# Performance work log

Measured on AMD Instinct MI355X. Metric: run time of the kernel, lower is better.

## Reference

```python
import jax, jax.numpy as jnp
import numpy as np

N_NODES = 50000
NUM_FEATURES = 256
HIDDEN_DIM = 64
N_EDGES = 1000000
NEG_SLOPE = 0.2  # PyG GATConv default negative_slope
EPS = 1e-16      # PyG softmax denominator epsilon


def gat_conv(x, src, dst, W, a_src, a_dst, bias, num_nodes):
    """Single-head PyG-style GATConv with self-loops already included in (src, dst).

    x: [N, F_in]; W: [F_in, F_out]; a_src/a_dst: [F_out]; bias: [F_out].
    """
    h = x @ W                                   # [N, F_out]
    alpha_src = h @ a_src                       # [N]
    alpha_dst = h @ a_dst                       # [N]
    e = alpha_src[src] + alpha_dst[dst]         # [E]
    e = jnp.where(e >= 0, e, NEG_SLOPE * e)     # LeakyReLU
    # segment softmax over incoming edges of each destination node
    m = jax.ops.segment_max(e, dst, num_segments=num_nodes)   # [N]
    e = jnp.exp(e - m[dst])                                    # [E]
    s = jax.ops.segment_sum(e, dst, num_segments=num_nodes)   # [N]
    alpha = e / (s[dst] + EPS)                                 # [E]
    out = jax.ops.segment_sum(alpha[:, None] * h[src], dst, num_segments=num_nodes)
    return out + bias


def setup_inputs() -> dict:
    key = jax.random.key(0)
    ks = jax.random.split(key, 12)
    glorot = lambda k, shp: jax.random.normal(k, shp, jnp.float32) * np.sqrt(2.0 / sum(shp))
    return {
        "x": jax.random.normal(ks[0], (N_NODES, NUM_FEATURES), jnp.float32),
        "edge_index": jax.random.randint(ks[1], (2, N_EDGES), 0, N_NODES, jnp.int64),
        "W1": glorot(ks[2], (NUM_FEATURES, HIDDEN_DIM)),
        "a1_src": glorot(ks[3], (HIDDEN_DIM,)),
        "a1_dst": glorot(ks[4], (HIDDEN_DIM,)),
        "b1": jnp.zeros((HIDDEN_DIM,), jnp.float32),
        "W2": glorot(ks[5], (HIDDEN_DIM, HIDDEN_DIM)),
        "a2_src": glorot(ks[6], (HIDDEN_DIM,)),
        "a2_dst": glorot(ks[7], (HIDDEN_DIM,)),
        "b2": jnp.zeros((HIDDEN_DIM,), jnp.float32),
        "fc_w": glorot(ks[8], (2 * HIDDEN_DIM, 1)),
        "fc_b": jnp.zeros((1,), jnp.float32),
    }


def reference(x, edge_index, W1, a1_src, a1_dst, b1, W2, a2_src, a2_dst, b2, fc_w, fc_b):
    num_nodes = x.shape[0]
    src_e, dst_e = edge_index[0], edge_index[1]
    # PyG GATConv adds self-loops by default
    loops = jnp.arange(num_nodes, dtype=edge_index.dtype)
    src = jnp.concatenate([src_e, loops])
    dst = jnp.concatenate([dst_e, loops])

    h = jax.nn.relu(gat_conv(x, src, dst, W1, a1_src, a1_dst, b1, num_nodes))
    h = jax.nn.relu(gat_conv(h, src, dst, W2, a2_src, a2_dst, b2, num_nodes))

    # edge-wise rating prediction on the ORIGINAL edges (no self-loops)
    combined = jnp.concatenate([h[src_e], h[dst_e]], axis=1)  # [E, 2*hidden]
    return combined @ fc_w + fc_b                              # [E, 1]
```

## Files before the change

### kernel.cpp

```cpp
#include <hip/hip_runtime.h>
#include <hip/hip_bf16.h>
#include <hip/hip_fp16.h>

#define NEG_SLOPE 0.2f
#define SEPS 1e-16f
#define CAP 64
#define NB 128
#define BSHIFT 9
#define CH 4096

using f16x8 = __attribute__((ext_vector_type(8))) _Float16;
using f32x4 = __attribute__((ext_vector_type(4))) float;

template <int K, bool HALF_IN>
__device__ __forceinline__ void gemm_body(char* smem, const void* __restrict__ Xv,
                                          const float* __restrict__ W,
                                          const float* __restrict__ av,
                                          const float* __restrict__ bv,
                                          __half* __restrict__ Yh,
                                          float* __restrict__ oa,
                                          float* __restrict__ ob, int N, int bid) {
  constexpr int PITCH = 40;
  _Float16* Al  = (_Float16*)smem;
  _Float16* Btl = Al + 64 * PITCH;
  _Float16* Ep  = (_Float16*)smem;

  int tid = threadIdx.x;
  int wid = tid >> 6, lane = tid & 63;
  int g = lane >> 4, c = lane & 15;
  int row0 = bid * 64;
  int sr = tid >> 2, sq = tid & 3;
  int wk = tid >> 4, wq = tid & 15;
  bool arow_ok = (row0 + sr) < N;
  const char* aptr = HALF_IN ? (const char*)((const _Float16*)Xv + (size_t)(row0 + sr) * K + sq * 8)
                             : (const char*)((const float*)Xv + (size_t)(row0 + sr) * K + sq * 8);

  f32x4 acc[4];
#pragma unroll
  for (int n = 0; n < 4; ++n) acc[n] = f32x4{0.f, 0.f, 0.f, 0.f};

  auto loadA = [&](int kt) -> f16x8 {
    f16x8 h = {};
    if (arow_ok) {
      if (HALF_IN) {
        h = *(const f16x8*)(aptr + (size_t)kt * 2);
      } else {
        const float* xp = (const float*)(aptr + (size_t)kt * 4);
        float4 a = *(const float4*)xp;
        float4 b = *(const float4*)(xp + 4);
        h[0] = (_Float16)a.x; h[1] = (_Float16)a.y;
        h[2] = (_Float16)a.z; h[3] = (_Float16)a.w;
        h[4] = (_Float16)b.x; h[5] = (_Float16)b.y;
        h[6] = (_Float16)b.z; h[7] = (_Float16)b.w;
      }
    }
    return h;
  };

  f16x8 ha = loadA(0);
  float4 w0 = *(const float4*)&W[(size_t)wk * 64 + wq * 4];
  float4 w1 = *(const float4*)&W[(size_t)(wk + 16) * 64 + wq * 4];

  for (int kt = 0; kt < K; kt += 32) {
    *(f16x8*)&Al[sr * PITCH + sq * 8] = ha;
    Btl[(wq * 4 + 0) * PITCH + wk] = (_Float16)w0.x;
    Btl[(wq * 4 + 1) * PITCH + wk] = (_Float16)w0.y;
    Btl[(wq * 4 + 2) * PITCH + wk] = (_Float16)w0.z;
    Btl[(wq * 4 + 3) * PITCH + wk] = (_Float16)w0.w;
    Btl[(wq * 4 + 0) * PITCH + wk + 16] = (_Float16)w1.x;
    Btl[(wq * 4 + 1) * PITCH + wk + 16] = (_Float16)w1.y;
    Btl[(wq * 4 + 2) * PITCH + wk + 16] = (_Float16)w1.z;
    Btl[(wq * 4 + 3) * PITCH + wk + 16] = (_Float16)w1.w;
    __syncthreads();
    f16x8 ha_n = {};
    float4 w0_n, w1_n;
    if (kt + 32 < K) {
      ha_n = loadA(kt + 32);
      w0_n = *(const float4*)&W[(size_t)(kt + 32 + wk) * 64 + wq * 4];
      w1_n = *(const float4*)&W[(size_t)(kt + 32 + wk + 16) * 64 + wq * 4];
    }
    f16x8 af = *(f16x8*)&Al[(wid * 16 + c) * PITCH + g * 8];
#pragma unroll
    for (int n = 0; n < 4; ++n) {
      f16x8 bf = *(f16x8*)&Btl[(n * 16 + c) * PITCH + g * 8];
      acc[n] = __builtin_amdgcn_mfma_f32_16x16x32_f16(af, bf, acc[n], 0, 0, 0);
    }
    __syncthreads();
    ha = ha_n; w0 = w0_n; w1 = w1_n;
  }

  {
    float avc[4], bvc[4];
#pragma unroll
    for (int n = 0; n < 4; ++n) { avc[n] = av[n * 16 + c]; bvc[n] = bv[n * 16 + c]; }
#pragma unroll
    for (int r = 0; r < 4; ++r) {
      float pa = 0.f, pb = 0.f;
#pragma unroll
      for (int n = 0; n < 4; ++n) { pa += acc[n][r] * avc[n]; pb += acc[n][r] * bvc[n]; }
#pragma unroll
      for (int off = 1; off < 16; off <<= 1) {
        pa += __shfl_xor(pa, off);
        pb += __shfl_xor(pb, off);
      }
      int row = row0 + wid * 16 + g * 4 + r;
      if (c == 0 && row < N) { oa[row] = pa; ob[row] = pb; }
    }
  }

  __syncthreads();
#pragma unroll
  for (int n = 0; n < 4; ++n)
#pragma unroll
    for (int r = 0; r < 4; ++r)
      Ep[(wid * 16 + g * 4 + r) * 72 + n * 16 + c] = (_Float16)acc[n][r];
  __syncthreads();
  {
    int row = row0 + sr;
    if (row < N) {
      float4 v0 = *(float4*)&Ep[sr * 72 + sq * 8];
      float4 v1 = *(float4*)&Ep[sr * 72 + (sq + 4) * 8];
      ((float4*)(Yh + (size_t)row * 64))[sq] = v0;
      ((float4*)(Yh + (size_t)row * 64))[sq + 4] = v1;
    }
  }
}

__device__ __forceinline__ void partition_body(char* smem, const void* ei,
                                               unsigned* __restrict__ bdata,
                                               int* __restrict__ pbh,
                                               int* __restrict__ plofs,
                                               unsigned* __restrict__ epk,
                                               int* __restrict__ cnt,
                                               int E, int N, int NPB, int pb) {
  int* hist = (int*)smem;
  int* lofs = hist + NB;
  unsigned* stage = (unsigned*)(lofs + NB);
  int* s_is64 = (int*)(stage + CH);
  int tid = threadIdx.x;
  long long Etot = (long long)E + N;
  long long base = (long long)pb * CH;

  for (int i = pb * 256 + tid; i < N; i += NPB * 256) cnt[i] = 0;
  if (tid < 64) {
    unsigned hi = ((const unsigned*)ei)[2 * tid + 1];
    unsigned long long m = __ballot(hi != 0);
    if (tid == 0) *s_is64 = (m == 0ULL) ? 1 : 0;
  }
  for (int i = tid; i < NB; i += 256) hist[i] = 0;
  __syncthreads();
  int f = *s_is64;

  unsigned sd[16];
  int lp[16], bk[16];
#pragma unroll
  for (int k = 0; k < 16; ++k) {
    long long i = base + tid + k * 256;
    if (i < Etot) {
      int s, d;
      if (i < E) {
        s = f ? (int)((const long long*)ei)[i] : ((const int*)ei)[i];
        d = f ? (int)((const long long*)ei)[E + i] : ((const int*)ei)[E + i];
      } else {
        s = d = (int)(i - E);
      }
      sd[k] = ((unsigned)d << 16) | (unsigned)s;
      bk[k] = d >> BSHIFT;
      lp[k] = atomicAdd(&hist[bk[k]], 1);
      if (i < E) epk[i] = sd[k];
    } else {
      bk[k] = -1;
    }
  }
  __syncthreads();
  if (tid < 64) {
    int h0 = hist[2 * tid], h1 = hist[2 * tid + 1];
    int v = h0 + h1, incl = v;
#pragma unroll
    for (int off = 1; off < 64; off <<= 1) {
      int t = __shfl_up(incl, off);
      if (tid >= off) incl += t;
    }
    int excl = incl - v;
    lofs[2 * tid] = excl;
    lofs[2 * tid + 1] = excl + h0;
  }
  __syncthreads();
  if (tid < NB) {
    pbh[pb * NB + tid] = hist[tid];
    plofs[pb * NB + tid] = lofs[tid];
  }
#pragma unroll
  for (int k = 0; k < 16; ++k)
    if (bk[k] >= 0) stage[lofs[bk[k]] + lp[k]] = sd[k];
  __syncthreads();
  int cnt_here = (int)((Etot - base < CH) ? (Etot - base) : CH);
  for (int j = tid; j < cnt_here; j += 256) bdata[base + j] = stage[j];
}

__global__ __launch_bounds__(256) void fused_front(const float* __restrict__ x,
                                                   const float* __restrict__ W1,
                                                   const float* __restrict__ a1s,
                                                   const float* __restrict__ a1d,
                                                   __half* __restrict__ hA,
                                                   float* __restrict__ alpha_s,
                                                   float* __restrict__ alpha_d,
                                                   const void* ei, unsigned* __restrict__ bdata,
                                                   int* __restrict__ pbh, int* __restrict__ plofs,
                                                   unsigned* __restrict__ epk,
                                                   int* __restrict__ cnt,
                                                   int E, int N, int NPB, int GB) {
  __shared__ __align__(16) char smem[(NB + NB) * 4 + CH * 4 + 16];
  if ((int)blockIdx.x < GB)
    gemm_body<256, false>(smem, x, W1, a1s, a1d, hA, alpha_s, alpha_d, N, blockIdx.x);
  else
    partition_body(smem, ei, bdata, pbh, plofs, epk, cnt, E, N, NPB, blockIdx.x - GB);
}

template <int K, bool HALF_IN>
__global__ __launch_bounds__(256) void gemm_mfma(const void* __restrict__ Xv,
                                                 const float* __restrict__ W,
                                                 const float* __restrict__ av,
                                                 const float* __restrict__ bv,
                                                 __half* __restrict__ Yh,
                                                 float* __restrict__ oa,
                                                 float* __restrict__ ob, int N) {
  __shared__ __align__(16) char smem[10240];
  gemm_body<K, HALF_IN>(smem, Xv, W, av, bv, Yh, oa, ob, N, blockIdx.x);
}

__global__ void build_kernel(const int* __restrict__ pbh, const int* __restrict__ plofs,
                             const unsigned* __restrict__ bdata, int* __restrict__ cnt,
                             unsigned short* __restrict__ csr, int NPB, int nb) {
  int b = blockIdx.x >> 2, sub = blockIdx.x & 3;
  if (b >= nb) return;
  __shared__ int cbase[66];
  __shared__ int cstart[67];
  int tid = threadIdx.x;
  int nj = (NPB - sub + 3) >> 2;
  if (tid < nj) {
    int B = sub + 4 * tid;
    cbase[tid] = B * CH + plofs[B * NB + b];
    cstart[tid] = pbh[B * NB + b];
  }
  __syncthreads();
  if (tid == 0) {
    int acc = 0;
    for (int j = 0; j < nj; ++j) { int l = cstart[j]; cstart[j] = acc; acc += l; }
    cstart[nj] = acc;
  }
  __syncthreads();
  int T = cstart[nj];
  for (int fidx = tid; fidx < T; fidx += 256) {
    int lo = 0, hi = nj;
    while (hi - lo > 1) {
      int mid = (lo + hi) >> 1;
      if (cstart[mid] <= fidx) lo = mid; else hi = mid;
    }
    unsigned v = bdata[cbase[lo] + (fidx - cstart[lo])];
    int d = (int)(v >> 16);
    int pos = atomicAdd(&cnt[d], 1);
    if (pos < CAP) csr[(size_t)d * CAP + pos] = (unsigned short)(v & 0xFFFFu);
  }
}

__global__ void agg_kernel(const int* __restrict__ cnt, const unsigned short* __restrict__ csr,
                           const __half* __restrict__ H, const float* __restrict__ as_,
                           const float* __restrict__ ad_, const float* __restrict__ bias,
                           __half* __restrict__ out, int N,
                           const float* __restrict__ pw,
                           float* __restrict__ pout, float* __restrict__ qout) {
  int node = (int)((blockIdx.x * blockDim.x + threadIdx.x) >> 6);
  int lane = threadIdx.x & 63;
  if (node >= N) return;
  int deg = cnt[node];
  deg = (deg > CAP) ? CAP : deg;
  const unsigned short* row = csr + (size_t)node * CAP;
  float ad = ad_[node];
  int g = lane >> 3, fl = lane & 7;
  int nj = (deg > g) ? ((deg - g + 7) >> 3) : 0;
  const float4* H16 = (const float4*)H;

  int sv[8];
#pragma unroll
  for (int j = 0; j < 8; ++j) sv[j] = row[j * 8 + g];
  float ev[8];
  float4 raw[8];
#pragma unroll
  for (int j = 0; j < 8; ++j)
    if (j < nj) ev[j] = as_[sv[j]];
#pragma unroll
  for (int j = 0; j < 8; ++j)
    if (j < nj) raw[j] = H16[(size_t)sv[j] * 8 + fl];

  float a[8];
#pragma unroll
  for (int k = 0; k < 8; ++k) a[k] = 0.f;
  float ss = 0.f;
#pragma unroll
  for (int j = 0; j < 8; ++j) {
    if (j < nj) {
      float e = ev[j] + ad;
      e = (e >= 0.f) ? e : NEG_SLOPE * e;
      float p = __expf(e);
      ss += p;
      float2 f0 = __half22float2(*(__half2*)&raw[j].x);
      float2 f1 = __half22float2(*(__half2*)&raw[j].y);
      float2 f2 = __half22float2(*(__half2*)&raw[j].z);
      float2 f3 = __half22float2(*(__half2*)&raw[j].w);
      a[0] += p * f0.x; a[1] += p * f0.y;
      a[2] += p * f1.x; a[3] += p * f1.y;
      a[4] += p * f2.x; a[5] += p * f2.y;
      a[6] += p * f3.x; a[7] += p * f3.y;
    }
  }
#pragma unroll
  for (int off = 8; off <= 32; off <<= 1) {
#pragma unroll
    for (int k = 0; k < 8; ++k) a[k] += __shfl_xor(a[k], off);
    ss += __shfl_xor(ss, off);
  }
  float inv = 1.f / (ss + SEPS);
  float o[8];
#pragma unroll
  for (int k = 0; k < 8; ++k) o[k] = fmaxf(a[k] * inv + bias[8 * fl + k], 0.f);
  if (g == 0) {
    if (out) {
      float4 packed;
      *(__half2*)&packed.x = __floats2half2_rn(o[0], o[1]);
      *(__half2*)&packed.y = __floats2half2_rn(o[2], o[3]);
      *(__half2*)&packed.z = __floats2half2_rn(o[4], o[5]);
      *(__half2*)&packed.w = __floats2half2_rn(o[6], o[7]);
      ((float4*)out)[(size_t)node * 8 + fl] = packed;
    }
    if (pw) {
      float pp = 0.f, qq = 0.f;
#pragma unroll
      for (int k = 0; k < 8; ++k) {
        pp += o[k] * pw[8 * fl + k];
        qq += o[k] * pw[64 + 8 * fl + k];
      }
#pragma unroll
      for (int off = 1; off < 8; off <<= 1) {
        pp += __shfl_xor(pp, off);
        qq += __shfl_xor(qq, off);
      }
      if (fl == 0) { pout[node] = pp; qout[node] = qq; }
    }
  }
}

__global__ void final_kernel(const unsigned* __restrict__ epk,
                             const float* __restrict__ p, const float* __restrict__ q,
                             const float* __restrict__ fcb, float* __restrict__ out,
                             int E, long long T) {
  long long t = (long long)blockIdx.x * blockDim.x + threadIdx.x;
  if (t >= T) return;
  float c = fcb[0];
#pragma unroll
  for (int k = 0; k < 4; ++k) {
    long long i = t + (long long)k * T;
    if (i < E) {
      unsigned v = epk[i];
      out[i] = p[v & 0xFFFFu] + q[v >> 16] + c;
    }
  }
}

extern "C" void kernel_launch(void* const* d_in, const int* in_sizes, int n_in,
                              void* d_out, int out_size, void* d_ws, size_t ws_size,
                              hipStream_t stream) {
  const float* x   = (const float*)d_in[0];
  const void*  ei  = d_in[1];
  const float* W1  = (const float*)d_in[2];
  const float* a1s = (const float*)d_in[3];
  const float* a1d = (const float*)d_in[4];
  const float* b1  = (const float*)d_in[5];
  const float* W2  = (const float*)d_in[6];
  const float* a2s = (const float*)d_in[7];
  const float* a2d = (const float*)d_in[8];
  const float* b2  = (const float*)d_in[9];
  const float* fcw = (const float*)d_in[10];
  const float* fcb = (const float*)d_in[11];
  float* out = (float*)d_out;

  int N = in_sizes[0] / 256;
  int E = in_sizes[1] / 2;
  long long Etot = (long long)E + N;
  int nb = (N + ((1 << BSHIFT) - 1)) >> BSHIFT;
  int NPB = (int)((Etot + CH - 1) / CH);
  int GB = (N + 63) / 64;

  char* w = (char*)d_ws;
  auto alloc = [&](size_t bytes) {
    char* p = w;
    w += (bytes + 255) & ~(size_t)255;
    return p;
  };
  int*            cnt     = (int*)alloc((size_t)N * 4);
  unsigned*       bdata   = (unsigned*)alloc((size_t)NPB * CH * 4);
  int*            pbh     = (int*)alloc((size_t)NPB * NB * 4);
  int*            plofs   = (int*)alloc((size_t)NPB * NB * 4);
  unsigned*       epk     = (unsigned*)alloc((size_t)E * 4);
  unsigned short* csr     = (unsigned short*)alloc((size_t)N * CAP * 2);
  float*          alpha_s = (float*)alloc((size_t)N * 4);
  float*          alpha_d = (float*)alloc((size_t)N * 4);
  __half*         hA      = (__half*)alloc((size_t)N * 64 * 2);
  __half*         hB      = (__half*)alloc((size_t)N * 64 * 2);
  float*          pbuf    = (float*)alloc((size_t)N * 4);
  float*          qbuf    = (float*)alloc((size_t)N * 4);

  fused_front<<<GB + NPB, 256, 0, stream>>>(x, W1, a1s, a1d, hA, alpha_s, alpha_d,
                                            ei, bdata, pbh, plofs, epk, cnt, E, N, NPB, GB);
  build_kernel<<<nb * 4, 256, 0, stream>>>(pbh, plofs, bdata, cnt, csr, NPB, nb);
  agg_kernel<<<(N + 3) / 4, 256, 0, stream>>>(cnt, csr, hA, alpha_s, alpha_d, b1, hB, N,
                                              nullptr, nullptr, nullptr);
  gemm_mfma<64, true><<<GB, 256, 0, stream>>>(hB, W2, a2s, a2d, hA, alpha_s, alpha_d, N);
  agg_kernel<<<(N + 3) / 4, 256, 0, stream>>>(cnt, csr, hA, alpha_s, alpha_d, b2, nullptr, N,
                                              fcw, pbuf, qbuf);
  long long T4 = ((long long)E + 3) / 4;
  final_kernel<<<(int)((T4 + 255) / 256), 256, 0, stream>>>(epk, pbuf, qbuf, fcb, out, E, T4);
}
```

Baseline: 122.5 us.

## Fuse layer-1 aggregation with layer-2 GEMM and widen final kernel per-thread work

Layer-1 neighbour aggregation now writes each 64-node tile into shared memory, and the same block multiplies it by W2 with MFMA to produce layer-2 features and attention logits. This removes a kernel launch and the global write and read of the intermediate hidden features. Separate alpha buffers are added because the fused kernel reads the layer-1 logits while writing the layer-2 ones. The trade-off is lower parallelism: the fused kernel launches one block per 64 nodes, and each wave aggregates 16 nodes in sequence, which may hide gather latency less well. The final edge kernel also processes 8 edges per thread instead of 4.

Measured after the change: 127.7 us. +4.3%, slower.

```diff
diff --git a/kernel.cpp b/kernel.cpp
--- a/kernel.cpp
+++ b/kernel.cpp
@@ -217,18 +217,6 @@
     partition_body(smem, ei, bdata, pbh, plofs, epk, cnt, E, N, NPB, blockIdx.x - GB);
 }
 
-template <int K, bool HALF_IN>
-__global__ __launch_bounds__(256) void gemm_mfma(const void* __restrict__ Xv,
-                                                 const float* __restrict__ W,
-                                                 const float* __restrict__ av,
-                                                 const float* __restrict__ bv,
-                                                 __half* __restrict__ Yh,
-                                                 float* __restrict__ oa,
-                                                 float* __restrict__ ob, int N) {
-  __shared__ __align__(16) char smem[10240];
-  gemm_body<K, HALF_IN>(smem, Xv, W, av, bv, Yh, oa, ob, N, blockIdx.x);
-}
-
 __global__ void build_kernel(const int* __restrict__ pbh, const int* __restrict__ plofs,
                              const unsigned* __restrict__ bdata, int* __restrict__ cnt,
                              unsigned short* __restrict__ csr, int NPB, int nb) {
@@ -264,23 +252,14 @@
   }
 }
 
-__global__ void agg_kernel(const int* __restrict__ cnt, const unsigned short* __restrict__ csr,
-                           const __half* __restrict__ H, const float* __restrict__ as_,
-                           const float* __restrict__ ad_, const float* __restrict__ bias,
-                           __half* __restrict__ out, int N,
-                           const float* __restrict__ pw,
-                           float* __restrict__ pout, float* __restrict__ qout) {
-  int node = (int)((blockIdx.x * blockDim.x + threadIdx.x) >> 6);
-  int lane = threadIdx.x & 63;
-  if (node >= N) return;
-  int deg = cnt[node];
-  deg = (deg > CAP) ? CAP : deg;
-  const unsigned short* row = csr + (size_t)node * CAP;
-  float ad = ad_[node];
-  int g = lane >> 3, fl = lane & 7;
+__device__ __forceinline__ void agg_node(int node, int deg,
+                                         const unsigned short* __restrict__ row,
+                                         const __half* __restrict__ H,
+                                         const float* __restrict__ as_, float ad,
+                                         const float* __restrict__ bias,
+                                         int g, int fl, float* o) {
   int nj = (deg > g) ? ((deg - g + 7) >> 3) : 0;
   const float4* H16 = (const float4*)H;
-
   int sv[8];
 #pragma unroll
   for (int j = 0; j < 8; ++j) sv[j] = row[j * 8 + g];
@@ -321,32 +300,135 @@
     ss += __shfl_xor(ss, off);
   }
   float inv = 1.f / (ss + SEPS);
+#pragma unroll
+  for (int k = 0; k < 8; ++k) o[k] = fmaxf(a[k] * inv + bias[8 * fl + k], 0.f);
+}
+
+__global__ __launch_bounds__(256) void agg_gemm(const int* __restrict__ cnt,
+                                                const unsigned short* __restrict__ csr,
+                                                const __half* __restrict__ H,
+                                                const float* __restrict__ as_,
+                                                const float* __restrict__ ad_,
+                                                const float* __restrict__ b1,
+                                                const float* __restrict__ W2,
+                                                const float* __restrict__ a2s,
+                                                const float* __restrict__ a2d,
+                                                __half* __restrict__ hA2,
+                                                float* __restrict__ oa2,
+                                                float* __restrict__ ob2, int N) {
+  constexpr int PITCH = 72;
+  __shared__ __align__(16) _Float16 Atile[64 * PITCH];
+  __shared__ __align__(16) _Float16 Btl[64 * PITCH];
+  int tid = threadIdx.x;
+  int wid = tid >> 6, lane = tid & 63;
+  int g = lane >> 3, fl = lane & 7;
+  int g4 = lane >> 4, c = lane & 15;
+  int base = blockIdx.x * 64;
+  int wk = tid >> 4, wq = tid & 15;
+
+#pragma unroll
+  for (int kk = 0; kk < 64; kk += 16) {
+    float4 w = *(const float4*)&W2[(size_t)(kk + wk) * 64 + wq * 4];
+    Btl[(wq * 4 + 0) * PITCH + kk + wk] = (_Float16)w.x;
+    Btl[(wq * 4 + 1) * PITCH + kk + wk] = (_Float16)w.y;
+    Btl[(wq * 4 + 2) * PITCH + kk + wk] = (_Float16)w.z;
+    Btl[(wq * 4 + 3) * PITCH + kk + wk] = (_Float16)w.w;
+  }
+
+  for (int t = 0; t < 16; ++t) {
+    int node = base + wid * 16 + t;
+    int nd = (node < N) ? node : 0;
+    int deg = (node < N) ? cnt[nd] : 0;
+    deg = (deg > CAP) ? CAP : deg;
+    float ad = ad_[nd];
+    float o[8];
+    agg_node(nd, deg, csr + (size_t)nd * CAP, H, as_, ad, b1, g, fl, o);
+    if (g == 0) {
+      f16x8 h;
+#pragma unroll
+      for (int k = 0; k < 8; ++k) h[k] = (node < N) ? (_Float16)o[k] : (_Float16)0.f;
+      *(f16x8*)&Atile[(wid * 16 + t) * PITCH + fl * 8] = h;
+    }
+  }
+  __syncthreads();
+
+  f32x4 acc[4];
+#pragma unroll
+  for (int n = 0; n < 4; ++n) acc[n] = f32x4{0.f, 0.f, 0.f, 0.f};
+#pragma unroll
+  for (int kt = 0; kt < 64; kt += 32) {
+    f16x8 af = *(f16x8*)&Atile[(wid * 16 + c) * PITCH + kt + g4 * 8];
+#pragma unroll
+    for (int n = 0; n < 4; ++n) {
+      f16x8 bf = *(f16x8*)&Btl[(n * 16 + c) * PITCH + kt + g4 * 8];
+      acc[n] = __builtin_amdgcn_mfma_f32_16x16x32_f16(af, bf, acc[n], 0, 0, 0);
+    }
+  }
+
+  {
+    float avc[4], bvc[4];
+#pragma unroll
+    for (int n = 0; n < 4; ++n) { avc[n] = a2s[n * 16 + c]; bvc[n] = a2d[n * 16 + c]; }
+#pragma unroll
+    for (int r = 0; r < 4; ++r) {
+      float pa = 0.f, pb = 0.f;
+#pragma unroll
+      for (int n = 0; n < 4; ++n) { pa += acc[n][r] * avc[n]; pb += acc[n][r] * bvc[n]; }
+#pragma unroll
+      for (int off = 1; off < 16; off <<= 1) {
+        pa += __shfl_xor(pa, off);
+        pb += __shfl_xor(pb, off);
+      }
+      int row = base + wid * 16 + g4 * 4 + r;
+      if (c == 0 && row < N) { oa2[row] = pa; ob2[row] = pb; }
+    }
+  }
+
+  __syncthreads();
+#pragma unroll
+  for (int n = 0; n < 4; ++n)
+#pragma unroll
+    for (int r = 0; r < 4; ++r)
+      Atile[(wid * 16 + g4 * 4 + r) * PITCH + n * 16 + c] = (_Float16)acc[n][r];
+  __syncthreads();
+  {
+    int sr = tid >> 2, sq = tid & 3;
+    int row = base + sr;
+    if (row < N) {
+      float4 v0 = *(float4*)&Atile[sr * PITCH + sq * 8];
+      float4 v1 = *(float4*)&Atile[sr * PITCH + (sq + 4) * 8];
+      ((float4*)(hA2 + (size_t)row * 64))[sq] = v0;
+      ((float4*)(hA2 + (size_t)row * 64))[sq + 4] = v1;
+    }
+  }
+}
+
+__global__ void agg2_kernel(const int* __restrict__ cnt, const unsigned short* __restrict__ csr,
+                            const __half* __restrict__ H, const float* __restrict__ as_,
+                            const float* __restrict__ ad_, const float* __restrict__ bias,
+                            int N, const float* __restrict__ pw,
+                            float* __restrict__ pout, float* __restrict__ qout) {
+  int node = (int)((blockIdx.x * blockDim.x + threadIdx.x) >> 6);
+  int lane = threadIdx.x & 63;
+  if (node >= N) return;
+  int deg = cnt[node];
+  deg = (deg > CAP) ? CAP : deg;
+  int g = lane >> 3, fl = lane & 7;
   float o[8];
-#pragma unroll
-  for (int k = 0; k < 8; ++k) o[k] = fmaxf(a[k] * inv + bias[8 * fl + k], 0.f);
+  agg_node(node, deg, csr + (size_t)node * CAP, H, as_, ad_[node], bias, g, fl, o);
   if (g == 0) {
-    if (out) {
-      float4 packed;
-      *(__half2*)&packed.x = __floats2half2_rn(o[0], o[1]);
-      *(__half2*)&packed.y = __floats2half2_rn(o[2], o[3]);
-      *(__half2*)&packed.z = __floats2half2_rn(o[4], o[5]);
-      *(__half2*)&packed.w = __floats2half2_rn(o[6], o[7]);
-      ((float4*)out)[(size_t)node * 8 + fl] = packed;
-    }
-    if (pw) {
-      float pp = 0.f, qq = 0.f;
-#pragma unroll
-      for (int k = 0; k < 8; ++k) {
-        pp += o[k] * pw[8 * fl + k];
-        qq += o[k] * pw[64 + 8 * fl + k];
-      }
-#pragma unroll
-      for (int off = 1; off < 8; off <<= 1) {
-        pp += __shfl_xor(pp, off);
-        qq += __shfl_xor(qq, off);
-      }
-      if (fl == 0) { pout[node] = pp; qout[node] = qq; }
-    }
+    float pp = 0.f, qq = 0.f;
+#pragma unroll
+    for (int k = 0; k < 8; ++k) {
+      pp += o[k] * pw[8 * fl + k];
+      qq += o[k] * pw[64 + 8 * fl + k];
+    }
+#pragma unroll
+    for (int off = 1; off < 8; off <<= 1) {
+      pp += __shfl_xor(pp, off);
+      qq += __shfl_xor(qq, off);
+    }
+    if (fl == 0) { pout[node] = pp; qout[node] = qq; }
   }
 }
 
@@ -358,7 +440,7 @@
   if (t >= T) return;
   float c = fcb[0];
 #pragma unroll
-  for (int k = 0; k < 4; ++k) {
+  for (int k = 0; k < 8; ++k) {
     long long i = t + (long long)k * T;
     if (i < E) {
       unsigned v = epk[i];
@@ -397,27 +479,28 @@
     w += (bytes + 255) & ~(size_t)255;
     return p;
   };
-  int*            cnt     = (int*)alloc((size_t)N * 4);
-  unsigned*       bdata   = (unsigned*)alloc((size_t)NPB * CH * 4);
-  int*            pbh     = (int*)alloc((size_t)NPB * NB * 4);
-  int*            plofs   = (int*)alloc((size_t)NPB * NB * 4);
-  unsigned*       epk     = (unsigned*)alloc((size_t)E * 4);
-  unsigned short* csr     = (unsigned short*)alloc((size_t)N * CAP * 2);
-  float*          alpha_s = (float*)alloc((size_t)N * 4);
-  float*          alpha_d = (float*)alloc((size_t)N * 4);
-  __half*         hA      = (__half*)alloc((size_t)N * 64 * 2);
-  __half*         hB      = (__half*)alloc((size_t)N * 64 * 2);
-  float*          pbuf    = (float*)alloc((size_t)N * 4);
-  float*          qbuf    = (float*)alloc((size_t)N * 4);
+  int*            cnt      = (int*)alloc((size_t)N * 4);
+  unsigned*       bdata    = (unsigned*)alloc((size_t)NPB * CH * 4);
+  int*            pbh      = (int*)alloc((size_t)NPB * NB * 4);
+  int*            plofs    = (int*)alloc((size_t)NPB * NB * 4);
+  unsigned*       epk      = (unsigned*)alloc((size_t)E * 4);
+  unsigned short* csr      = (unsigned short*)alloc((size_t)N * CAP * 2);
+  float*          alpha_s  = (float*)alloc((size_t)N * 4);
+  float*          alpha_d  = (float*)alloc((size_t)N * 4);
+  float*          alpha_s2 = (float*)alloc((size_t)N * 4);
+  float*          alpha_d2 = (float*)alloc((size_t)N * 4);
+  __half*         hA       = (__half*)alloc((size_t)N * 64 * 2);
+  __half*         hA2      = (__half*)alloc((size_t)N * 64 * 2);
+  float*          pbuf     = (float*)alloc((size_t)N * 4);
+  float*          qbuf     = (float*)alloc((size_t)N * 4);
 
   fused_front<<<GB + NPB, 256, 0, stream>>>(x, W1, a1s, a1d, hA, alpha_s, alpha_d,
                                             ei, bdata, pbh, plofs, epk, cnt, E, N, NPB, GB);
   build_kernel<<<nb * 4, 256, 0, stream>>>(pbh, plofs, bdata, cnt, csr, NPB, nb);
-  agg_kernel<<<(N + 3) / 4, 256, 0, stream>>>(cnt, csr, hA, alpha_s, alpha_d, b1, hB, N,
-                                              nullptr, nullptr, nullptr);
-  gemm_mfma<64, true><<<GB, 256, 0, stream>>>(hB, W2, a2s, a2d, hA, alpha_s, alpha_d, N);
-  agg_kernel<<<(N + 3) / 4, 256, 0, stream>>>(cnt, csr, hA, alpha_s, alpha_d, b2, nullptr, N,
-                                              fcw, pbuf, qbuf);
-  long long T4 = ((long long)E + 3) / 4;
-  final_kernel<<<(int)((T4 + 255) / 256), 256, 0, stream>>>(epk, pbuf, qbuf, fcb, out, E, T4);
-}
+  agg_gemm<<<GB, 256, 0, stream>>>(cnt, csr, hA, alpha_s, alpha_d, b1, W2, a2s, a2d,
+                                   hA2, alpha_s2, alpha_d2, N);
+  agg2_kernel<<<(N + 3) / 4, 256, 0, stream>>>(cnt, csr, hA2, alpha_s2, alpha_d2, b2, N,
+                                               fcw, pbuf, qbuf);
+  long long T8 = ((long long)E + 7) / 8;
+  final_kernel<<<(int)((T8 + 255) / 256), 256, 0, stream>>>(epk, pbuf, qbuf, fcb, out, E, T8);
+}
```

## Build CSR with one block per bucket using LDS degree counters

Applied to the files above, without the earlier changes.

The CSR build kernel now runs one block per destination bucket of 512 nodes instead of four sub-blocks, and counts degrees with LDS atomics in place of global atomics on cnt. Each block writes the capped counts at the end, so the cnt zeroing in the partition blocks is removed. A wave-level scan replaces the serial prefix sum, and each thread issues four bdata loads before doing the atomics. Separately, layer-2 alpha values go to their own buffers and the final kernel handles eight edges per thread. The cost is fewer build blocks (about 98), so less parallelism, and NPB must stay within MAXNPB=320 with PER at most 8.

After: 129.3 us. 5.6% more time.

```diff
diff --git a/kernel.cpp b/kernel.cpp
--- a/kernel.cpp
+++ b/kernel.cpp
@@ -8,6 +8,7 @@
 #define NB 128
 #define BSHIFT 9
 #define CH 4096
+#define MAXNPB 320
 
 using f16x8 = __attribute__((ext_vector_type(8))) _Float16;
 using f32x4 = __attribute__((ext_vector_type(4))) float;
@@ -131,8 +132,7 @@
                                                int* __restrict__ pbh,
                                                int* __restrict__ plofs,
                                                unsigned* __restrict__ epk,
-                                               int* __restrict__ cnt,
-                                               int E, int N, int NPB, int pb) {
+                                               int E, int N, int pb) {
   int* hist = (int*)smem;
   int* lofs = hist + NB;
   unsigned* stage = (unsigned*)(lofs + NB);
@@ -141,7 +141,6 @@
   long long Etot = (long long)E + N;
   long long base = (long long)pb * CH;
 
-  for (int i = pb * 256 + tid; i < N; i += NPB * 256) cnt[i] = 0;
   if (tid < 64) {
     unsigned hi = ((const unsigned*)ei)[2 * tid + 1];
     unsigned long long m = __ballot(hi != 0);
@@ -208,13 +207,12 @@
                                                    const void* ei, unsigned* __restrict__ bdata,
                                                    int* __restrict__ pbh, int* __restrict__ plofs,
                                                    unsigned* __restrict__ epk,
-                                                   int* __restrict__ cnt,
-                                                   int E, int N, int NPB, int GB) {
+                                                   int E, int N, int GB) {
   __shared__ __align__(16) char smem[(NB + NB) * 4 + CH * 4 + 16];
   if ((int)blockIdx.x < GB)
     gemm_body<256, false>(smem, x, W1, a1s, a1d, hA, alpha_s, alpha_d, N, blockIdx.x);
   else
-    partition_body(smem, ei, bdata, pbh, plofs, epk, cnt, E, N, NPB, blockIdx.x - GB);
+    partition_body(smem, ei, bdata, pbh, plofs, epk, E, N, blockIdx.x - GB);
 }
 
 template <int K, bool HALF_IN>
@@ -229,58 +227,95 @@
   gemm_body<K, HALF_IN>(smem, Xv, W, av, bv, Yh, oa, ob, N, blockIdx.x);
 }
 
-__global__ void build_kernel(const int* __restrict__ pbh, const int* __restrict__ plofs,
-                             const unsigned* __restrict__ bdata, int* __restrict__ cnt,
-                             unsigned short* __restrict__ csr, int NPB, int nb) {
-  int b = blockIdx.x >> 2, sub = blockIdx.x & 3;
-  if (b >= nb) return;
-  __shared__ int cbase[66];
-  __shared__ int cstart[67];
+__global__ __launch_bounds__(256) void build_kernel(const int* __restrict__ pbh,
+                                                    const int* __restrict__ plofs,
+                                                    const unsigned* __restrict__ bdata,
+                                                    int* __restrict__ cnt,
+                                                    unsigned short* __restrict__ csr,
+                                                    int NPB, int N) {
+  int b = blockIdx.x;
+  __shared__ int cbase[MAXNPB];
+  __shared__ int cstart[MAXNPB + 1];
+  __shared__ int lcnt[1 << BSHIFT];
   int tid = threadIdx.x;
-  int nj = (NPB - sub + 3) >> 2;
-  if (tid < nj) {
-    int B = sub + 4 * tid;
-    cbase[tid] = B * CH + plofs[B * NB + b];
-    cstart[tid] = pbh[B * NB + b];
-  }
-  __syncthreads();
-  if (tid == 0) {
-    int acc = 0;
-    for (int j = 0; j < nj; ++j) { int l = cstart[j]; cstart[j] = acc; acc += l; }
-    cstart[nj] = acc;
-  }
-  __syncthreads();
-  int T = cstart[nj];
-  for (int fidx = tid; fidx < T; fidx += 256) {
-    int lo = 0, hi = nj;
-    while (hi - lo > 1) {
-      int mid = (lo + hi) >> 1;
-      if (cstart[mid] <= fidx) lo = mid; else hi = mid;
-    }
-    unsigned v = bdata[cbase[lo] + (fidx - cstart[lo])];
-    int d = (int)(v >> 16);
-    int pos = atomicAdd(&cnt[d], 1);
-    if (pos < CAP) csr[(size_t)d * CAP + pos] = (unsigned short)(v & 0xFFFFu);
-  }
-}
-
-__global__ void agg_kernel(const int* __restrict__ cnt, const unsigned short* __restrict__ csr,
-                           const __half* __restrict__ H, const float* __restrict__ as_,
-                           const float* __restrict__ ad_, const float* __restrict__ bias,
-                           __half* __restrict__ out, int N,
-                           const float* __restrict__ pw,
-                           float* __restrict__ pout, float* __restrict__ qout) {
-  int node = (int)((blockIdx.x * blockDim.x + threadIdx.x) >> 6);
-  int lane = threadIdx.x & 63;
-  if (node >= N) return;
-  int deg = cnt[node];
-  deg = (deg > CAP) ? CAP : deg;
-  const unsigned short* row = csr + (size_t)node * CAP;
-  float ad = ad_[node];
-  int g = lane >> 3, fl = lane & 7;
+  for (int j = tid; j < NPB; j += 256) {
+    cbase[j] = j * CH + plofs[j * NB + b];
+    cstart[j] = pbh[j * NB + b];
+  }
+  for (int i = tid; i < (1 << BSHIFT); i += 256) lcnt[i] = 0;
+  __syncthreads();
+  if (tid < 64) {
+    const int PER = (NPB + 63) >> 6;
+    int idx0 = tid * PER;
+    int vals[8];
+    int lsum = 0;
+#pragma unroll 5
+    for (int k = 0; k < PER; ++k) {
+      int id = idx0 + k;
+      int v = (id < NPB) ? cstart[id] : 0;
+      vals[k] = lsum;
+      lsum += v;
+    }
+    int incl = lsum;
+#pragma unroll
+    for (int off = 1; off < 64; off <<= 1) {
+      int t = __shfl_up(incl, off);
+      if (tid >= off) incl += t;
+    }
+    int excl = incl - lsum;
+#pragma unroll 5
+    for (int k = 0; k < PER; ++k) {
+      int id = idx0 + k;
+      if (id < NPB) cstart[id] = excl + vals[k];
+    }
+    if (tid == 63) cstart[NPB] = incl;
+  }
+  __syncthreads();
+  int T = cstart[NPB];
+  int dbase = b << BSHIFT;
+  for (int it = tid; it < T; it += 1024) {
+    unsigned v[4];
+    int ok[4];
+#pragma unroll
+    for (int k = 0; k < 4; ++k) {
+      int fidx = it + k * 256;
+      ok[k] = fidx < T;
+      if (ok[k]) {
+        int lo = 0, hi = NPB;
+        while (hi - lo > 1) {
+          int mid = (lo + hi) >> 1;
+          if (cstart[mid] <= fidx) lo = mid; else hi = mid;
+        }
+        v[k] = bdata[cbase[lo] + (fidx - cstart[lo])];
+      }
+    }
+#pragma unroll
+    for (int k = 0; k < 4; ++k) {
+      if (ok[k]) {
+        int d = (int)(v[k] >> 16);
+        int pos = atomicAdd(&lcnt[d - dbase], 1);
+        if (pos < CAP) csr[(size_t)d * CAP + pos] = (unsigned short)(v[k] & 0xFFFFu);
+      }
+    }
+  }
+  __syncthreads();
+  for (int i = tid; i < (1 << BSHIFT); i += 256) {
+    int node = dbase + i;
+    if (node < N) {
+      int c = lcnt[i];
+      cnt[node] = (c > CAP) ? CAP : c;
+    }
+  }
+}
+
+__device__ __forceinline__ void agg_node(int deg,
+                                         const unsigned short* __restrict__ row,
+                                         const __half* __restrict__ H,
+                                         const float* __restrict__ as_, float ad,
+                                         const float* __restrict__ bias,
+                                         int g, int fl, float* o) {
   int nj = (deg > g) ? ((deg - g + 7) >> 3) : 0;
   const float4* H16 = (const float4*)H;
-
   int sv[8];
 #pragma unroll
   for (int j = 0; j < 8; ++j) sv[j] = row[j * 8 + g];
@@ -321,9 +356,23 @@
     ss += __shfl_xor(ss, off);
   }
   float inv = 1.f / (ss + SEPS);
+#pragma unroll
+  for (int k = 0; k < 8; ++k) o[k] = fmaxf(a[k] * inv + bias[8 * fl + k], 0.f);
+}
+
+__global__ void agg_kernel(const int* __restrict__ cnt, const unsigned short* __restrict__ csr,
+                           const __half* __restrict__ H, const float* __restrict__ as_,
+                           const float* __restrict__ ad_, const float* __restrict__ bias,
+                           __half* __restrict__ out, int N,
+                           const float* __restrict__ pw,
+                           float* __restrict__ pout, float* __restrict__ qout) {
+  int node = (int)((blockIdx.x * blockDim.x + threadIdx.x) >> 6);
+  int lane = threadIdx.x & 63;
+  if (node >= N) return;
+  int deg = cnt[node];
+  int g = lane >> 3, fl = lane & 7;
   float o[8];
-#pragma unroll
-  for (int k = 0; k < 8; ++k) o[k] = fmaxf(a[k] * inv + bias[8 * fl + k], 0.f);
+  agg_node(deg, csr + (size_t)node * CAP, H, as_, ad_[node], bias, g, fl, o);
   if (g == 0) {
     if (out) {
       float4 packed;
@@ -358,7 +407,7 @@
   if (t >= T) return;
   float c = fcb[0];
 #pragma unroll
-  for (int k = 0; k < 4; ++k) {
+  for (int k = 0; k < 8; ++k) {
     long long i = t + (long long)k * T;
     if (i < E) {
       unsigned v = epk[i];
@@ -397,27 +446,29 @@
     w += (bytes + 255) & ~(size_t)255;
     return p;
   };
-  int*            cnt     = (int*)alloc((size_t)N * 4);
-  unsigned*       bdata   = (unsigned*)alloc((size_t)NPB * CH * 4);
-  int*            pbh     = (int*)alloc((size_t)NPB * NB * 4);
-  int*            plofs   = (int*)alloc((size_t)NPB * NB * 4);
-  unsigned*       epk     = (unsigned*)alloc((size_t)E * 4);
-  unsigned short* csr     = (unsigned short*)alloc((size_t)N * CAP * 2);
-  float*          alpha_s = (float*)alloc((size_t)N * 4);
-  float*          alpha_d = (float*)alloc((size_t)N * 4);
-  __half*         hA      = (__half*)alloc((size_t)N * 64 * 2);
-  __half*         hB      = (__half*)alloc((size_t)N * 64 * 2);
-  float*          pbuf    = (float*)alloc((size_t)N * 4);
-  float*          qbuf    = (float*)alloc((size_t)N * 4);
+  int*            cnt      = (int*)alloc((size_t)N * 4);
+  unsigned*       bdata    = (unsigned*)alloc((size_t)NPB * CH * 4);
+  int*            pbh      = (int*)alloc((size_t)NPB * NB * 4);
+  int*            plofs    = (int*)alloc((size_t)NPB * NB * 4);
+  unsigned*       epk      = (unsigned*)alloc((size_t)E * 4);
+  unsigned short* csr      = (unsigned short*)alloc((size_t)N * CAP * 2);
+  float*          alpha_s  = (float*)alloc((size_t)N * 4);
+  float*          alpha_d  = (float*)alloc((size_t)N * 4);
+  float*          alpha_s2 = (float*)alloc((size_t)N * 4);
+  float*          alpha_d2 = (float*)alloc((size_t)N * 4);
+  __half*         hA       = (__half*)alloc((size_t)N * 64 * 2);
+  __half*         hB       = (__half*)alloc((size_t)N * 64 * 2);
+  float*          pbuf     = (float*)alloc((size_t)N * 4);
+  float*          qbuf     = (float*)alloc((size_t)N * 4);
 
   fused_front<<<GB + NPB, 256, 0, stream>>>(x, W1, a1s, a1d, hA, alpha_s, alpha_d,
-                                            ei, bdata, pbh, plofs, epk, cnt, E, N, NPB, GB);
-  build_kernel<<<nb * 4, 256, 0, stream>>>(pbh, plofs, bdata, cnt, csr, NPB, nb);
+                                            ei, bdata, pbh, plofs, epk, E, N, GB);
+  build_kernel<<<nb, 256, 0, stream>>>(pbh, plofs, bdata, cnt, csr, NPB, N);
   agg_kernel<<<(N + 3) / 4, 256, 0, stream>>>(cnt, csr, hA, alpha_s, alpha_d, b1, hB, N,
                                               nullptr, nullptr, nullptr);
-  gemm_mfma<64, true><<<GB, 256, 0, stream>>>(hB, W2, a2s, a2d, hA, alpha_s, alpha_d, N);
-  agg_kernel<<<(N + 3) / 4, 256, 0, stream>>>(cnt, csr, hA, alpha_s, alpha_d, b2, nullptr, N,
+  gemm_mfma<64, true><<<GB, 256, 0, stream>>>(hB, W2, a2s, a2d, hA, alpha_s2, alpha_d2, N);
+  agg_kernel<<<(N + 3) / 4, 256, 0, stream>>>(cnt, csr, hA, alpha_s2, alpha_d2, b2, nullptr, N,
                                               fcw, pbuf, qbuf);
-  long long T4 = ((long long)E + 3) / 4;
-  final_kernel<<<(int)((T4 + 255) / 256), 256, 0, stream>>>(epk, pbuf, qbuf, fcb, out, E, T4);
-}
+  long long T8 = ((long long)E + 7) / 8;
+  final_kernel<<<(int)((T8 + 255) / 256), 256, 0, stream>>>(epk, pbuf, qbuf, fcb, out, E, T8);
+}
```

## Split node features into two 32-wide half planes and restructure aggregation per plane

Applied to the files above, without the earlier changes.

Node feature matrices are now stored as two planes of 32 halves each (columns 0-31, then 32-63), written by the GEMM epilogue and read plane by plane in the aggregation kernel. The aggregation kernel now maps 16 edge groups of 4 lanes, loads the CSR row with ushort4 vector loads, and computes softmax weights once before gathering each plane. This is meant to make each gathered row segment smaller and more cache-friendly and to cut shuffle work. It also gives the second layer separate alpha buffers and has the final kernel handle 8 edges per thread. The cost is two passes of gathers and reductions per node.

Measured after the change: 173.1 us. 41.4% more time.

```diff
diff --git a/kernel.cpp b/kernel.cpp
--- a/kernel.cpp
+++ b/kernel.cpp
@@ -11,6 +11,7 @@
 
 using f16x8 = __attribute__((ext_vector_type(8))) _Float16;
 using f32x4 = __attribute__((ext_vector_type(4))) float;
+
 
 template <int K, bool HALF_IN>
 __device__ __forceinline__ void gemm_body(char* smem, const void* __restrict__ Xv,
@@ -32,8 +33,8 @@
   int sr = tid >> 2, sq = tid & 3;
   int wk = tid >> 4, wq = tid & 15;
   bool arow_ok = (row0 + sr) < N;
-  const char* aptr = HALF_IN ? (const char*)((const _Float16*)Xv + (size_t)(row0 + sr) * K + sq * 8)
-                             : (const char*)((const float*)Xv + (size_t)(row0 + sr) * K + sq * 8);
+  const float*    aptrF = (const float*)Xv + (size_t)(row0 + sr) * K + sq * 8;
+  const _Float16* aptrH = (const _Float16*)Xv + (size_t)(row0 + sr) * 32 + sq * 8;
 
   f32x4 acc[4];
 #pragma unroll
@@ -43,9 +44,9 @@
     f16x8 h = {};
     if (arow_ok) {
       if (HALF_IN) {
-        h = *(const f16x8*)(aptr + (size_t)kt * 2);
+        h = *(const f16x8*)(aptrH + (kt >= 32 ? (size_t)N * 32 : 0));
       } else {
-        const float* xp = (const float*)(aptr + (size_t)kt * 4);
+        const float* xp = aptrF + kt;
         float4 a = *(const float4*)xp;
         float4 b = *(const float4*)(xp + 4);
         h[0] = (_Float16)a.x; h[1] = (_Float16)a.y;
@@ -120,8 +121,8 @@
     if (row < N) {
       float4 v0 = *(float4*)&Ep[sr * 72 + sq * 8];
       float4 v1 = *(float4*)&Ep[sr * 72 + (sq + 4) * 8];
-      ((float4*)(Yh + (size_t)row * 64))[sq] = v0;
-      ((float4*)(Yh + (size_t)row * 64))[sq + 4] = v1;
+      ((float4*)(Yh + (size_t)row * 32))[sq] = v0;
+      ((float4*)(Yh + (size_t)N * 32 + (size_t)row * 32))[sq] = v1;
     }
   }
 }
@@ -265,7 +266,8 @@
 }
 
 __global__ void agg_kernel(const int* __restrict__ cnt, const unsigned short* __restrict__ csr,
-                           const __half* __restrict__ H, const float* __restrict__ as_,
+                           const __half* __restrict__ H,
+                           const float* __restrict__ as_,
                            const float* __restrict__ ad_, const float* __restrict__ bias,
                            __half* __restrict__ out, int N,
                            const float* __restrict__ pw,
@@ -277,76 +279,83 @@
   deg = (deg > CAP) ? CAP : deg;
   const unsigned short* row = csr + (size_t)node * CAP;
   float ad = ad_[node];
-  int g = lane >> 3, fl = lane & 7;
-  int nj = (deg > g) ? ((deg - g + 7) >> 3) : 0;
-  const float4* H16 = (const float4*)H;
-
-  int sv[8];
-#pragma unroll
-  for (int j = 0; j < 8; ++j) sv[j] = row[j * 8 + g];
-  float ev[8];
-  float4 raw[8];
-#pragma unroll
-  for (int j = 0; j < 8; ++j)
-    if (j < nj) ev[j] = as_[sv[j]];
-#pragma unroll
-  for (int j = 0; j < 8; ++j)
-    if (j < nj) raw[j] = H16[(size_t)sv[j] * 8 + fl];
-
-  float a[8];
-#pragma unroll
-  for (int k = 0; k < 8; ++k) a[k] = 0.f;
+  int g = lane >> 2, fl = lane & 3;
+  int nj = deg - g * 4;
+  nj = nj < 0 ? 0 : (nj > 4 ? 4 : nj);
+
+  ushort4 sv4 = *(const ushort4*)&row[g * 4];
+  int sv[4] = {sv4.x, sv4.y, sv4.z, sv4.w};
+
+  float p[4];
   float ss = 0.f;
 #pragma unroll
-  for (int j = 0; j < 8; ++j) {
+  for (int j = 0; j < 4; ++j) {
     if (j < nj) {
-      float e = ev[j] + ad;
+      float e = as_[sv[j]] + ad;
       e = (e >= 0.f) ? e : NEG_SLOPE * e;
-      float p = __expf(e);
-      ss += p;
-      float2 f0 = __half22float2(*(__half2*)&raw[j].x);
-      float2 f1 = __half22float2(*(__half2*)&raw[j].y);
-      float2 f2 = __half22float2(*(__half2*)&raw[j].z);
-      float2 f3 = __half22float2(*(__half2*)&raw[j].w);
-      a[0] += p * f0.x; a[1] += p * f0.y;
-      a[2] += p * f1.x; a[3] += p * f1.y;
-      a[4] += p * f2.x; a[5] += p * f2.y;
-      a[6] += p * f3.x; a[7] += p * f3.y;
-    }
-  }
-#pragma unroll
-  for (int off = 8; off <= 32; off <<= 1) {
-#pragma unroll
-    for (int k = 0; k < 8; ++k) a[k] += __shfl_xor(a[k], off);
-    ss += __shfl_xor(ss, off);
-  }
+      p[j] = __expf(e);
+      ss += p[j];
+    } else {
+      p[j] = 0.f;
+    }
+  }
+#pragma unroll
+  for (int off = 4; off <= 32; off <<= 1) ss += __shfl_xor(ss, off);
   float inv = 1.f / (ss + SEPS);
-  float o[8];
-#pragma unroll
-  for (int k = 0; k < 8; ++k) o[k] = fmaxf(a[k] * inv + bias[8 * fl + k], 0.f);
-  if (g == 0) {
-    if (out) {
+
+  float pp = 0.f, qq = 0.f;
+#pragma unroll
+  for (int h = 0; h < 2; ++h) {
+    const float4* H16 = (const float4*)(H + (size_t)h * N * 32);
+    float4 raw[4];
+#pragma unroll
+    for (int j = 0; j < 4; ++j)
+      if (j < nj) raw[j] = H16[(size_t)sv[j] * 4 + fl];
+    float a[8];
+#pragma unroll
+    for (int k = 0; k < 8; ++k) a[k] = 0.f;
+#pragma unroll
+    for (int j = 0; j < 4; ++j) {
+      if (j < nj) {
+        float2 f0 = __half22float2(*(__half2*)&raw[j].x);
+        float2 f1 = __half22float2(*(__half2*)&raw[j].y);
+        float2 f2 = __half22float2(*(__half2*)&raw[j].z);
+        float2 f3 = __half22float2(*(__half2*)&raw[j].w);
+        a[0] += p[j] * f0.x; a[1] += p[j] * f0.y;
+        a[2] += p[j] * f1.x; a[3] += p[j] * f1.y;
+        a[4] += p[j] * f2.x; a[5] += p[j] * f2.y;
+        a[6] += p[j] * f3.x; a[7] += p[j] * f3.y;
+      }
+    }
+#pragma unroll
+    for (int off = 4; off <= 32; off <<= 1) {
+#pragma unroll
+      for (int k = 0; k < 8; ++k) a[k] += __shfl_xor(a[k], off);
+    }
+    float o[8];
+#pragma unroll
+    for (int k = 0; k < 8; ++k)
+      o[k] = fmaxf(a[k] * inv + bias[h * 32 + fl * 8 + k], 0.f);
+    if (out && g == 0) {
       float4 packed;
       *(__half2*)&packed.x = __floats2half2_rn(o[0], o[1]);
       *(__half2*)&packed.y = __floats2half2_rn(o[2], o[3]);
       *(__half2*)&packed.z = __floats2half2_rn(o[4], o[5]);
       *(__half2*)&packed.w = __floats2half2_rn(o[6], o[7]);
-      ((float4*)out)[(size_t)node * 8 + fl] = packed;
+      ((float4*)(out + (size_t)h * N * 32 + (size_t)node * 32))[fl] = packed;
     }
     if (pw) {
-      float pp = 0.f, qq = 0.f;
 #pragma unroll
       for (int k = 0; k < 8; ++k) {
-        pp += o[k] * pw[8 * fl + k];
-        qq += o[k] * pw[64 + 8 * fl + k];
+        pp += o[k] * pw[h * 32 + fl * 8 + k];
+        qq += o[k] * pw[64 + h * 32 + fl * 8 + k];
       }
-#pragma unroll
-      for (int off = 1; off < 8; off <<= 1) {
-        pp += __shfl_xor(pp, off);
-        qq += __shfl_xor(qq, off);
-      }
-      if (fl == 0) { pout[node] = pp; qout[node] = qq; }
-    }
+    }
+  }
+  if (pw) {
+    pp += __shfl_xor(pp, 1); pp += __shfl_xor(pp, 2);
+    qq += __shfl_xor(qq, 1); qq += __shfl_xor(qq, 2);
+    if (lane == 0) { pout[node] = pp; qout[node] = qq; }
   }
 }
 
@@ -358,7 +367,7 @@
   if (t >= T) return;
   float c = fcb[0];
 #pragma unroll
-  for (int k = 0; k < 4; ++k) {
+  for (int k = 0; k < 8; ++k) {
     long long i = t + (long long)k * T;
     if (i < E) {
       unsigned v = epk[i];
@@ -397,27 +406,29 @@
     w += (bytes + 255) & ~(size_t)255;
     return p;
   };
-  int*            cnt     = (int*)alloc((size_t)N * 4);
-  unsigned*       bdata   = (unsigned*)alloc((size_t)NPB * CH * 4);
-  int*            pbh     = (int*)alloc((size_t)NPB * NB * 4);
-  int*            plofs   = (int*)alloc((size_t)NPB * NB * 4);
-  unsigned*       epk     = (unsigned*)alloc((size_t)E * 4);
-  unsigned short* csr     = (unsigned short*)alloc((size_t)N * CAP * 2);
-  float*          alpha_s = (float*)alloc((size_t)N * 4);
-  float*          alpha_d = (float*)alloc((size_t)N * 4);
-  __half*         hA      = (__half*)alloc((size_t)N * 64 * 2);
-  __half*         hB      = (__half*)alloc((size_t)N * 64 * 2);
-  float*          pbuf    = (float*)alloc((size_t)N * 4);
-  float*          qbuf    = (float*)alloc((size_t)N * 4);
+  int*            cnt      = (int*)alloc((size_t)N * 4);
+  unsigned*       bdata    = (unsigned*)alloc((size_t)NPB * CH * 4);
+  int*            pbh      = (int*)alloc((size_t)NPB * NB * 4);
+  int*            plofs    = (int*)alloc((size_t)NPB * NB * 4);
+  unsigned*       epk      = (unsigned*)alloc((size_t)E * 4);
+  unsigned short* csr      = (unsigned short*)alloc((size_t)N * CAP * 2);
+  float*          alpha_s  = (float*)alloc((size_t)N * 4);
+  float*          alpha_d  = (float*)alloc((size_t)N * 4);
+  float*          alpha_s2 = (float*)alloc((size_t)N * 4);
+  float*          alpha_d2 = (float*)alloc((size_t)N * 4);
+  __half*         hA       = (__half*)alloc((size_t)N * 64 * 2);
+  __half*         hB       = (__half*)alloc((size_t)N * 64 * 2);
+  float*          pbuf     = (float*)alloc((size_t)N * 4);
+  float*          qbuf     = (float*)alloc((size_t)N * 4);
 
   fused_front<<<GB + NPB, 256, 0, stream>>>(x, W1, a1s, a1d, hA, alpha_s, alpha_d,
                                             ei, bdata, pbh, plofs, epk, cnt, E, N, NPB, GB);
   build_kernel<<<nb * 4, 256, 0, stream>>>(pbh, plofs, bdata, cnt, csr, NPB, nb);
   agg_kernel<<<(N + 3) / 4, 256, 0, stream>>>(cnt, csr, hA, alpha_s, alpha_d, b1, hB, N,
                                               nullptr, nullptr, nullptr);
-  gemm_mfma<64, true><<<GB, 256, 0, stream>>>(hB, W2, a2s, a2d, hA, alpha_s, alpha_d, N);
-  agg_kernel<<<(N + 3) / 4, 256, 0, stream>>>(cnt, csr, hA, alpha_s, alpha_d, b2, nullptr, N,
+  gemm_mfma<64, true><<<GB, 256, 0, stream>>>(hB, W2, a2s, a2d, hA, alpha_s2, alpha_d2, N);
+  agg_kernel<<<(N + 3) / 4, 256, 0, stream>>>(cnt, csr, hA, alpha_s2, alpha_d2, b2, nullptr, N,
                                               fcw, pbuf, qbuf);
-  long long T4 = ((long long)E + 3) / 4;
-  final_kernel<<<(int)((T4 + 255) / 256), 256, 0, stream>>>(epk, pbuf, qbuf, fcb, out, E, T4);
-}
+  long long T8 = ((long long)E + 7) / 8;
+  final_kernel<<<(int)((T8 + 255) / 256), 256, 0, stream>>>(epk, pbuf, qbuf, fcb, out, E, T8);
+}
```
